# Performance work log

Measured on AMD Instinct MI355X. Metric: run time of the kernel, lower is better.

Reference implementation:

```python
import jax, jax.numpy as jnp
import numpy as np

NUM_HEADS = 16
HEAD_DIM = 64
D_MODEL = 1024
OUTPUT_DIM = 1024


def setup_inputs() -> dict:
    key = jax.random.key(0)
    ks = jax.random.split(key, 11)
    B, S, H = 2, 2048, D_MODEL
    inner = NUM_HEADS * HEAD_DIM
    s = 0.02
    return {
        "query": jax.random.normal(ks[0], (B, S, H), jnp.float32),
        "key": jax.random.normal(ks[1], (B, S, H), jnp.float32),
        "value": jax.random.normal(ks[2], (B, S, H), jnp.float32),
        "Wq": jax.random.normal(ks[3], (H, inner), jnp.float32) * s,
        "bq": jnp.zeros((inner,), jnp.float32),
        "Wk": jax.random.normal(ks[4], (H, inner), jnp.float32) * s,
        "bk": jnp.zeros((inner,), jnp.float32),
        "Wv": jax.random.normal(ks[5], (H, inner), jnp.float32) * s,
        "bv": jnp.zeros((inner,), jnp.float32),
        "Wo": jax.random.normal(ks[6], (inner, OUTPUT_DIM), jnp.float32) * s,
        "bo": jnp.zeros((OUTPUT_DIM,), jnp.float32),
    }


def reference(query, key, value, Wq, bq, Wk, bk, Wv, bv, Wo, bo):
    B, Sq, _ = query.shape
    Sk = key.shape[1]
    nh, dh = NUM_HEADS, HEAD_DIM
    # projections -> [B, S, nh, dh]
    Q = (query @ Wq + bq).reshape(B, Sq, nh, dh)
    K = (key @ Wk + bk).reshape(B, Sk, nh, dh)
    V = (value @ Wv + bv).reshape(B, Sk, nh, dh)
    # scores [B, nh, Sq, Sk]
    scores = jnp.einsum("bqhd,bkhd->bhqk", Q, K) / jnp.sqrt(jnp.float32(dh))
    attn = jax.nn.softmax(scores, axis=-1)
    out = jnp.einsum("bhqk,bkhd->bqhd", attn, V).reshape(B, Sq, nh * dh)
    return out @ Wo + bo
```

## Files before the change

kernel.cpp:

```cpp
#include <hip/hip_runtime.h>
#include <math.h>

typedef __attribute__((ext_vector_type(8))) short short8;
typedef __attribute__((ext_vector_type(4))) short short4v;
typedef __attribute__((ext_vector_type(4))) float f32x4;
typedef __attribute__((ext_vector_type(2))) float f32x2;

#if __has_builtin(__builtin_amdgcn_mfma_f32_16x16x16bf16_1k)
#define HAVE_MFMA16 1
#else
#define HAVE_MFMA16 0
#endif

__device__ __forceinline__ short f2bf(float f) {
  union { float f; unsigned u; } x; x.f = f;
  unsigned r = x.u + 0x7fffu + ((x.u >> 16) & 1u);
  return (short)(r >> 16);
}
#if __has_builtin(__builtin_amdgcn_cvt_pk_bf16_f32)
typedef __attribute__((ext_vector_type(2))) __bf16 bf16x2;
__device__ __forceinline__ unsigned pack_bf(float a, float b) {
  union { bf16x2 v; unsigned u; } t;
  t.v = __builtin_amdgcn_cvt_pk_bf16_f32(a, b);
  return t.u;
}
#else
__device__ __forceinline__ unsigned pack_bf(float a, float b) {
  union { float f; unsigned u; } x, y; x.f = a; y.f = b;
  unsigned ra = x.u + 0x7fffu + ((x.u >> 16) & 1u);
  unsigned rb = y.u + 0x7fffu + ((y.u >> 16) & 1u);
  return (ra >> 16) | (rb & 0xffff0000u);
}
#endif
__device__ __forceinline__ float fast_exp2(float x) {
#if __has_builtin(__builtin_amdgcn_exp2f)
  return __builtin_amdgcn_exp2f(x);
#else
  return exp2f(x);
#endif
}
union U4S8 { unsigned u[4]; short8 s; };
union U2S4 { unsigned u[2]; short4v s; };

__global__ __launch_bounds__(256) void wconv(
    const float* __restrict__ W0, const float* __restrict__ W1,
    const float* __restrict__ W2, const float* __restrict__ W3,
    short* __restrict__ T0, short* __restrict__ T1,
    short* __restrict__ T2, short* __restrict__ T3) {
  const float* W; short* T;
  switch (blockIdx.z) {
    case 0: W = W0; T = T0; break;
    case 1: W = W1; T = T1; break;
    case 2: W = W2; T = T2; break;
    default: W = W3; T = T3; break;
  }
  __shared__ __align__(16) short t[64][72];
  const int tid = threadIdx.x;
  const int x0 = blockIdx.x * 64, y0 = blockIdx.y * 64;
  {
    int rr = tid >> 2, cc = (tid & 3) * 16;
    const float* p = W + (size_t)(x0 + rr) * 1024 + y0 + cc;
    f32x4 v[4];
    v[0] = *(const f32x4*)(p + 0);  v[1] = *(const f32x4*)(p + 4);
    v[2] = *(const f32x4*)(p + 8);  v[3] = *(const f32x4*)(p + 12);
#pragma unroll
    for (int i = 0; i < 4; ++i)
#pragma unroll
      for (int j = 0; j < 4; ++j)
        t[cc + 4 * i + j][rr] = f2bf(v[i][j]);
  }
  __syncthreads();
  {
    int nr = tid >> 2, kc = (tid & 3) * 16;
    short* q = T + (size_t)(y0 + nr) * 1024 + x0 + kc;
    *(short8*)q       = *(const short8*)&t[nr][kc];
    *(short8*)(q + 8) = *(const short8*)&t[nr][kc + 8];
  }
}

template <bool A_IS_F32, bool B_IS_BF16, bool OUT_F32, int BM>
__global__ __launch_bounds__(256) void gemm_bias(
    const void* __restrict__ A0, const void* __restrict__ A1, const void* __restrict__ A2,
    const void* __restrict__ B0, const void* __restrict__ B1, const void* __restrict__ B2,
    const float* __restrict__ b0, const float* __restrict__ b1, const float* __restrict__ b2,
    void* __restrict__ C0, void* __restrict__ C1, void* __restrict__ C2,
    float s0, float s1, float s2, int M, int N, int K) {
  const int z = blockIdx.z;
  const void*  Av   = z == 0 ? A0 : (z == 1 ? A1 : A2);
  const void*  Bv   = z == 0 ? B0 : (z == 1 ? B1 : B2);
  const float* bias = z == 0 ? b0 : (z == 1 ? b1 : b2);
  void*        Cv   = z == 0 ? C0 : (z == 1 ? C1 : C2);
  const float  cs   = z == 0 ? s0 : (z == 1 ? s1 : s2);

  constexpr int MF = BM / 32;
  __shared__ __align__(16) short As[BM * 40];
  __shared__ __align__(16) short Bs[128 * 40];
  const int tid = threadIdx.x;
  const int l = tid & 63, w = tid >> 6;
  const int lr = l & 15, lq = l >> 4;
  const int lin = blockIdx.x + (int)gridDim.x * blockIdx.y;
  const int ny = (int)gridDim.y;
  const int yb = lin % ny, xb = lin / ny;
  const int m0 = yb * BM, n0 = xb * 128;
  const int wm = (w >> 1) * (BM / 2), wn = (w & 1) * 64;
  f32x4 acc[MF][4] = {};

  constexpr int TPR = 256 / BM;
  const int ar = tid / TPR, ac = (tid % TPR) * (32 / TPR);
  const int br = tid >> 1, bcc = (tid & 1) * 16;
  const int dp = tid & 63, kb = tid >> 6;

  f32x4 avf[MF];
  short8 avb[BM / 64 > 0 ? BM / 64 : 1];
  short8 bvb[2];
  f32x2 bvf[8];

  auto load_regs = [&](int k0) {
    if constexpr (A_IS_F32) {
      const float* Ap = (const float*)Av + (size_t)(m0 + ar) * K + k0 + ac;
#pragma unroll
      for (int i = 0; i < MF; ++i) avf[i] = *(const f32x4*)(Ap + 4 * i);
    } else {
      const short* Ap = (const short*)Av + (size_t)(m0 + ar) * K + k0 + ac;
#pragma unroll
      for (int i = 0; i < BM / 64; ++i) avb[i] = *(const short8*)(Ap + 8 * i);
    }
    if constexpr (B_IS_BF16) {
      const short* Bp = (const short*)Bv + (size_t)(n0 + br) * K + k0 + bcc;
      bvb[0] = *(const short8*)(Bp + 0);
      bvb[1] = *(const short8*)(Bp + 8);
    } else {
      const float* Bp = (const float*)Bv + (size_t)(k0 + kb * 8) * N + n0 + 2 * dp;
#pragma unroll
      for (int i = 0; i < 4; ++i) {
        bvf[2 * i]     = *(const f32x2*)(Bp + (size_t)(2 * i) * N);
        bvf[2 * i + 1] = *(const f32x2*)(Bp + (size_t)(2 * i + 1) * N);
      }
    }
  };
  auto write_lds = [&]() {
    if constexpr (A_IS_F32) {
#pragma unroll
      for (int j = 0; j < MF / 2; ++j) {
        U4S8 p;
        p.u[0] = pack_bf(avf[2 * j][0], avf[2 * j][1]);
        p.u[1] = pack_bf(avf[2 * j][2], avf[2 * j][3]);
        p.u[2] = pack_bf(avf[2 * j + 1][0], avf[2 * j + 1][1]);
        p.u[3] = pack_bf(avf[2 * j + 1][2], avf[2 * j + 1][3]);
        *(short8*)&As[ar * 40 + ac + 8 * j] = p.s;
      }
    } else {
#pragma unroll
      for (int j = 0; j < BM / 64; ++j)
        *(short8*)&As[ar * 40 + ac + 8 * j] = avb[j];
    }
    if constexpr (B_IS_BF16) {
      *(short8*)&Bs[br * 40 + bcc] = bvb[0];
      *(short8*)&Bs[br * 40 + bcc + 8] = bvb[1];
    } else {
      U4S8 lo, hi;
#pragma unroll
      for (int i = 0; i < 4; ++i) {
        lo.u[i] = pack_bf(bvf[2 * i][0], bvf[2 * i + 1][0]);
        hi.u[i] = pack_bf(bvf[2 * i][1], bvf[2 * i + 1][1]);
      }
      *(short8*)&Bs[(2 * dp) * 40 + kb * 8] = lo.s;
      *(short8*)&Bs[(2 * dp + 1) * 40 + kb * 8] = hi.s;
    }
  };

  load_regs(0);
  const int KT = K >> 5;
  for (int kt = 0; kt < KT; ++kt) {
    write_lds();
    __syncthreads();
    if (kt + 1 < KT) load_regs((kt + 1) * 32);

    short8 af[MF], bfr[4];
#pragma unroll
    for (int i = 0; i < MF; ++i)
      af[i] = *(const short8*)&As[(wm + i * 16 + lr) * 40 + lq * 8];
#pragma unroll
    for (int i = 0; i < 4; ++i)
      bfr[i] = *(const short8*)&Bs[(wn + i * 16 + lr) * 40 + lq * 8];
#pragma unroll
    for (int mi = 0; mi < MF; ++mi)
#pragma unroll
      for (int ni = 0; ni < 4; ++ni)
        acc[mi][ni] = __builtin_amdgcn_mfma_f32_16x16x32_bf16(af[mi], bfr[ni], acc[mi][ni], 0, 0, 0);
    __syncthreads();
  }

#pragma unroll
  for (int ni = 0; ni < 4; ++ni) {
    int gn = n0 + wn + ni * 16 + lr;
    float bv = bias[gn];
#pragma unroll
    for (int mi = 0; mi < MF; ++mi) {
      int gm = m0 + wm + mi * 16 + lq * 4;
#pragma unroll
      for (int r = 0; r < 4; ++r) {
        float val = (acc[mi][ni][r] + bv) * cs;
        if constexpr (OUT_F32)
          ((float*)Cv)[(size_t)(gm + r) * N + gn] = val;
        else
          ((short*)Cv)[(size_t)(gm + r) * N + gn] = f2bf(val);
      }
    }
  }
}

__global__ __launch_bounds__(256) void attn128(
    const short* __restrict__ Q, const short* __restrict__ K,
    const short* __restrict__ V, short* __restrict__ ctx) {
  __shared__ __align__(16) short Ks[64][72];
  __shared__ __align__(16) short Vt[64][72];
#if !HAVE_MFMA16
  __shared__ __align__(16) short Ps2[4][32][68];
#endif
  const int tid = threadIdx.x, l = tid & 63, w = tid >> 6;
  const int lr = l & 15, lq = l >> 4;
  const int lin = blockIdx.x + 16 * blockIdx.y;
  const int h = lin & 15, qblk = lin >> 4;
  const int b = blockIdx.z, q0 = qblk * 128;
  const size_t bh = (size_t)b * 2048 * 1024 + (size_t)h * 64;
  const short* Kg = K + bh;
  const short* Vg = V + bh;

  short8 qb[2][2];
#pragma unroll
  for (int qf = 0; qf < 2; ++qf)
#pragma unroll
    for (int ks = 0; ks < 2; ++ks)
      qb[qf][ks] = *(const short8*)&Q[bh + (size_t)(q0 + w * 32 + qf * 16 + lr) * 1024 + ks * 32 + lq * 8];

  f32x4 accO[4][2] = {};
  float lpart[2] = {0.f, 0.f};

  const int kr = tid >> 2, kc = (tid & 3) * 16;
  const int vdp = tid & 31, vkb = tid >> 5;

  short8 kv0, kv1;
  unsigned vu[8];
  auto load_kv = [&](int kt) {
    const short* Kp = &Kg[(size_t)(kt * 64 + kr) * 1024 + kc];
    kv0 = *(const short8*)(Kp + 0);
    kv1 = *(const short8*)(Kp + 8);
#pragma unroll
    for (int i = 0; i < 8; ++i)
      vu[i] = *(const unsigned*)&Vg[(size_t)(kt * 64 + vkb * 8 + i) * 1024 + vdp * 2];
  };
  auto write_kv = [&]() {
    *(short8*)&Ks[kr][kc] = kv0;
    *(short8*)&Ks[kr][kc + 8] = kv1;
    U4S8 lo, hi;
#pragma unroll
    for (int j = 0; j < 4; ++j) {
      lo.u[j] = (vu[2 * j] & 0xffffu) | (vu[2 * j + 1] << 16);
      hi.u[j] = (vu[2 * j] >> 16) | (vu[2 * j + 1] & 0xffff0000u);
    }
    *(short8*)&Vt[2 * vdp][vkb * 8] = lo.s;
    *(short8*)&Vt[2 * vdp + 1][vkb * 8] = hi.s;
  };

  load_kv(0);
  for (int kt = 0; kt < 32; ++kt) {
    write_kv();
    __syncthreads();
    if (kt + 1 < 32) load_kv(kt + 1);

    short8 ka[4][2];
#pragma unroll
    for (int ni = 0; ni < 4; ++ni)
#pragma unroll
      for (int ks = 0; ks < 2; ++ks)
        ka[ni][ks] = *(const short8*)&Ks[ni * 16 + lr][ks * 32 + lq * 8];
    f32x4 s[4][2] = {};
#pragma unroll
    for (int ni = 0; ni < 4; ++ni)
#pragma unroll
      for (int qf = 0; qf < 2; ++qf) {
        s[ni][qf] = __builtin_amdgcn_mfma_f32_16x16x32_bf16(ka[ni][0], qb[qf][0], s[ni][qf], 0, 0, 0);
        s[ni][qf] = __builtin_amdgcn_mfma_f32_16x16x32_bf16(ka[ni][1], qb[qf][1], s[ni][qf], 0, 0, 0);
      }

    unsigned pk[4][2][2];
#pragma unroll
    for (int ni = 0; ni < 4; ++ni)
#pragma unroll
      for (int qf = 0; qf < 2; ++qf) {
        float p0 = fast_exp2(s[ni][qf][0]);
        float p1 = fast_exp2(s[ni][qf][1]);
        float p2 = fast_exp2(s[ni][qf][2]);
        float p3 = fast_exp2(s[ni][qf][3]);
        lpart[qf] += (p0 + p1) + (p2 + p3);
        pk[ni][qf][0] = pack_bf(p0, p1);
        pk[ni][qf][1] = pack_bf(p2, p3);
      }

#if HAVE_MFMA16
#pragma unroll
    for (int di = 0; di < 4; ++di)
#pragma unroll
      for (int ni = 0; ni < 4; ++ni) {
        short4v vb = *(const short4v*)&Vt[di * 16 + lr][ni * 16 + lq * 4];
#pragma unroll
        for (int qf = 0; qf < 2; ++qf) {
          U2S4 a; a.u[0] = pk[ni][qf][0]; a.u[1] = pk[ni][qf][1];
          accO[di][qf] = __builtin_amdgcn_mfma_f32_16x16x16bf16_1k(a.s, vb, accO[di][qf], 0, 0, 0);
        }
      }
#else
#pragma unroll
    for (int ni = 0; ni < 4; ++ni)
#pragma unroll
      for (int qf = 0; qf < 2; ++qf) {
        unsigned* dst = (unsigned*)&Ps2[w][qf * 16 + lr][16 * ni + 4 * lq];
        dst[0] = pk[ni][qf][0];
        dst[1] = pk[ni][qf][1];
      }
#pragma unroll
    for (int ks = 0; ks < 2; ++ks)
#pragma unroll
      for (int qf = 0; qf < 2; ++qf) {
        const short* src = &Ps2[w][qf * 16 + lr][32 * ks + 8 * lq];
        U4S8 a;
        a.u[0] = ((const unsigned*)src)[0]; a.u[1] = ((const unsigned*)src)[1];
        a.u[2] = ((const unsigned*)src)[2]; a.u[3] = ((const unsigned*)src)[3];
#pragma unroll
        for (int di = 0; di < 4; ++di) {
          short8 vb = *(const short8*)&Vt[di * 16 + lr][ks * 32 + lq * 8];
          accO[di][qf] = __builtin_amdgcn_mfma_f32_16x16x32_bf16(a.s, vb, accO[di][qf], 0, 0, 0);
        }
      }
#endif
    __syncthreads();
  }

#pragma unroll
  for (int qf = 0; qf < 2; ++qf) {
    lpart[qf] += __shfl_xor(lpart[qf], 16, 64);
    lpart[qf] += __shfl_xor(lpart[qf], 32, 64);
  }
  float inv[2] = {1.0f / lpart[0], 1.0f / lpart[1]};
  float ir[2][4];
#pragma unroll
  for (int qf = 0; qf < 2; ++qf)
#pragma unroll
    for (int r = 0; r < 4; ++r)
      ir[qf][r] = __shfl(inv[qf], 4 * lq + r, 64);

#pragma unroll
  for (int qf = 0; qf < 2; ++qf)
#pragma unroll
    for (int r = 0; r < 4; ++r) {
      size_t row = bh + (size_t)(q0 + w * 32 + qf * 16 + 4 * lq + r) * 1024;
#pragma unroll
      for (int di = 0; di < 4; ++di)
        ctx[row + di * 16 + lr] = f2bf(accO[di][qf][r] * ir[qf][r]);
    }
}

extern "C" void kernel_launch(void* const* d_in, const int* in_sizes, int n_in,
                              void* d_out, int out_size, void* d_ws, size_t ws_size,
                              hipStream_t stream) {
  const void*  query = d_in[0];
  const void*  key   = d_in[1];
  const void*  value = d_in[2];
  const float* Wq = (const float*)d_in[3];
  const float* bq = (const float*)d_in[4];
  const float* Wk = (const float*)d_in[5];
  const float* bk = (const float*)d_in[6];
  const float* Wv = (const float*)d_in[7];
  const float* bv = (const float*)d_in[8];
  const float* Wo = (const float*)d_in[9];
  const float* bo = (const float*)d_in[10];

  short* ws = (short*)d_ws;
  const size_t MT = 4096ull * 1024ull;
  const size_t WSZ = 1024ull * 1024ull;
  short* Qb = ws;
  short* Vb = ws + MT;
  short* Kb = (short*)d_out;

  const bool roomy = ws_size >= (2 * MT + 4 * WSZ) * sizeof(short);
  short *WqT, *WkT, *WvT, *WoT;
  if (roomy) {
    short* base = ws + 2 * MT;
    WqT = base; WkT = base + WSZ; WvT = base + 2 * WSZ; WoT = base + 3 * WSZ;
  } else {
    short* tail = (short*)d_out + MT;
    WqT = tail; WkT = tail + WSZ; WvT = tail + 2 * WSZ; WoT = nullptr;
  }

  wconv<<<dim3(16, 16, roomy ? 4 : 3), 256, 0, stream>>>(
      Wq, Wk, Wv, Wo, WqT, WkT, WvT, roomy ? WoT : WvT);

  const float qscale = 0.125f * 1.4426950408889634f;
  gemm_bias<true, true, false, 128><<<dim3(8, 32, 3), 256, 0, stream>>>(
      query, key, value, WqT, WkT, WvT, bq, bk, bv, Qb, Kb, Vb,
      qscale, 1.0f, 1.0f, 4096, 1024, 1024);

  attn128<<<dim3(16, 16, 2), 256, 0, stream>>>(Qb, Kb, Vb, Qb );

  if (roomy)
    gemm_bias<false, true, true, 64><<<dim3(8, 64, 1), 256, 0, stream>>>(
        Qb, Qb, Qb, WoT, WoT, WoT, bo, bo, bo, d_out, d_out, d_out,
        1.0f, 1.0f, 1.0f, 4096, 1024, 1024);
  else
    gemm_bias<false, false, true, 64><<<dim3(8, 64, 1), 256, 0, stream>>>(
        Qb, Qb, Qb, Wo, Wo, Wo, bo, bo, bo, d_out, d_out, d_out,
        1.0f, 1.0f, 1.0f, 4096, 1024, 1024);
}
```

Measured before the change: 253.5 us.

## Pre-convert activations to bf16 and use async global-to-LDS GEMM loads

When the workspace is large enough, a new pass converts the query, key and value activations from fp32 to bf16 up front. New GEMMs then stream bf16 tiles straight from global memory into LDS using global_load_lds and run 16x16x32 bf16 MFMAs. The goal is to remove the per-tile fp32 conversion and register staging from the projection GEMM's inner loop. The cost is an extra launch and extra traffic to write and re-read bf16 copies of the activations, and the loop is still single-buffered with two barriers per k-step.

```diff
diff --git a/kernel.cpp b/kernel.cpp
--- a/kernel.cpp
+++ b/kernel.cpp
@@ -41,6 +41,12 @@
 }
 union U4S8 { unsigned u[4]; short8 s; };
 union U2S4 { unsigned u[2]; short4v s; };
+
+__device__ __forceinline__ void async16(const short* g, short* lds_uniform) {
+  __builtin_amdgcn_global_load_lds(
+      (const __attribute__((address_space(1))) void*)g,
+      (__attribute__((address_space(3))) void*)lds_uniform, 16, 0, 0);
+}
 
 __global__ __launch_bounds__(256) void wconv(
     const float* __restrict__ W0, const float* __restrict__ W1,
@@ -75,6 +81,118 @@
     short* q = T + (size_t)(y0 + nr) * 1024 + x0 + kc;
     *(short8*)q       = *(const short8*)&t[nr][kc];
     *(short8*)(q + 8) = *(const short8*)&t[nr][kc + 8];
+  }
+}
+
+__global__ __launch_bounds__(256) void aconv(
+    const float* __restrict__ X0, const float* __restrict__ X1, const float* __restrict__ X2,
+    short* __restrict__ Y0, short* __restrict__ Y1, short* __restrict__ Y2) {
+  const float* X; short* Y;
+  switch (blockIdx.z) {
+    case 0: X = X0; Y = Y0; break;
+    case 1: X = X1; Y = Y1; break;
+    default: X = X2; Y = Y2; break;
+  }
+  size_t idx = ((size_t)blockIdx.x * 256 + threadIdx.x) * 16;
+  f32x4 v0 = *(const f32x4*)(X + idx + 0);
+  f32x4 v1 = *(const f32x4*)(X + idx + 4);
+  f32x4 v2 = *(const f32x4*)(X + idx + 8);
+  f32x4 v3 = *(const f32x4*)(X + idx + 12);
+  U4S8 a, b;
+  a.u[0] = pack_bf(v0[0], v0[1]); a.u[1] = pack_bf(v0[2], v0[3]);
+  a.u[2] = pack_bf(v1[0], v1[1]); a.u[3] = pack_bf(v1[2], v1[3]);
+  b.u[0] = pack_bf(v2[0], v2[1]); b.u[1] = pack_bf(v2[2], v2[3]);
+  b.u[2] = pack_bf(v3[0], v3[1]); b.u[3] = pack_bf(v3[2], v3[3]);
+  *(short8*)(Y + idx) = a.s;
+  *(short8*)(Y + idx + 8) = b.s;
+}
+
+template <bool OUT_F32, int BM>
+__global__ __launch_bounds__(256) void gemm_async(
+    const short* __restrict__ A0, const short* __restrict__ A1, const short* __restrict__ A2,
+    const short* __restrict__ B0, const short* __restrict__ B1, const short* __restrict__ B2,
+    const float* __restrict__ b0, const float* __restrict__ b1, const float* __restrict__ b2,
+    void* __restrict__ C0, void* __restrict__ C1, void* __restrict__ C2,
+    float s0, float s1, float s2, int M, int N, int K) {
+  const int z = blockIdx.z;
+  const short* A    = z == 0 ? A0 : (z == 1 ? A1 : A2);
+  const short* B    = z == 0 ? B0 : (z == 1 ? B1 : B2);
+  const float* bias = z == 0 ? b0 : (z == 1 ? b1 : b2);
+  void*        Cv   = z == 0 ? C0 : (z == 1 ? C1 : C2);
+  const float  cs   = z == 0 ? s0 : (z == 1 ? s1 : s2);
+
+  constexpr int MF = BM / 32;
+  constexpr int AJ = BM / 64;
+  __shared__ __align__(16) short As[BM * 32];
+  __shared__ __align__(16) short Bs[128 * 32];
+  const int tid = threadIdx.x;
+  const int l = tid & 63, w = tid >> 6;
+  const int lr = l & 15, lq = l >> 4;
+  const int lin = blockIdx.x + (int)gridDim.x * blockIdx.y;
+  const int ny = (int)gridDim.y;
+  const int yb = lin % ny, xb = lin / ny;
+  const int m0 = yb * BM, n0 = xb * 128;
+  const int wm = (w >> 1) * (BM / 2), wn = (w & 1) * 64;
+  f32x4 acc[MF][4] = {};
+
+  const int lrow = l >> 2, lcol = (l & 3) * 8;
+  const short* aptr[AJ];
+  short* alds[AJ];
+#pragma unroll
+  for (int j = 0; j < AJ; ++j) {
+    int chunk = w * AJ + j;
+    aptr[j] = A + (size_t)(m0 + chunk * 16 + lrow) * K + lcol;
+    alds[j] = &As[chunk * 512];
+  }
+  const short* bptr[2];
+  short* blds[2];
+#pragma unroll
+  for (int j = 0; j < 2; ++j) {
+    int chunk = w * 2 + j;
+    bptr[j] = B + (size_t)(n0 + chunk * 16 + lrow) * K + lcol;
+    blds[j] = &Bs[chunk * 512];
+  }
+
+  const int KT = K >> 5;
+  for (int kt = 0; kt < KT; ++kt) {
+    const int k0 = kt * 32;
+    __syncthreads();
+#pragma unroll
+    for (int j = 0; j < AJ; ++j) async16(aptr[j] + k0, alds[j]);
+#pragma unroll
+    for (int j = 0; j < 2; ++j) async16(bptr[j] + k0, blds[j]);
+    __syncthreads();
+
+    short8 af[MF], bfr[4];
+#pragma unroll
+    for (int i = 0; i < MF; ++i)
+      af[i] = *(const short8*)&As[(wm + i * 16 + lr) * 32 + lq * 8];
+#pragma unroll
+    for (int i = 0; i < 4; ++i)
+      bfr[i] = *(const short8*)&Bs[(wn + i * 16 + lr) * 32 + lq * 8];
+#pragma unroll
+    for (int mi = 0; mi < MF; ++mi)
+#pragma unroll
+      for (int ni = 0; ni < 4; ++ni)
+        acc[mi][ni] = __builtin_amdgcn_mfma_f32_16x16x32_bf16(af[mi], bfr[ni], acc[mi][ni], 0, 0, 0);
+  }
+
+#pragma unroll
+  for (int ni = 0; ni < 4; ++ni) {
+    int gn = n0 + wn + ni * 16 + lr;
+    float bv = bias[gn];
+#pragma unroll
+    for (int mi = 0; mi < MF; ++mi) {
+      int gm = m0 + wm + mi * 16 + lq * 4;
+#pragma unroll
+      for (int r = 0; r < 4; ++r) {
+        float val = (acc[mi][ni][r] + bv) * cs;
+        if constexpr (OUT_F32)
+          ((float*)Cv)[(size_t)(gm + r) * N + gn] = val;
+        else
+          ((short*)Cv)[(size_t)(gm + r) * N + gn] = f2bf(val);
+      }
+    }
   }
 }
 
@@ -379,9 +497,35 @@
   short* ws = (short*)d_ws;
   const size_t MT = 4096ull * 1024ull;
   const size_t WSZ = 1024ull * 1024ull;
+  const float qscale = 0.125f * 1.4426950408889634f;
+
   short* Qb = ws;
   short* Vb = ws + MT;
   short* Kb = (short*)d_out;
+
+  const bool turbo = ws_size >= (4 * MT + 4 * WSZ) * sizeof(short);
+
+  if (turbo) {
+    short* Qcv = ws + 2 * MT;
+    short* Vcv = ws + 3 * MT;
+    short* Kcv = (short*)d_out + MT;
+    short* WqT = ws + 4 * MT;
+    short* WkT = WqT + WSZ;
+    short* WvT = WqT + 2 * WSZ;
+    short* WoT = WqT + 3 * WSZ;
+
+    wconv<<<dim3(16, 16, 4), 256, 0, stream>>>(Wq, Wk, Wv, Wo, WqT, WkT, WvT, WoT);
+    aconv<<<dim3(1024, 1, 3), 256, 0, stream>>>(
+        (const float*)query, (const float*)key, (const float*)value, Qcv, Kcv, Vcv);
+    gemm_async<false, 128><<<dim3(8, 32, 3), 256, 0, stream>>>(
+        Qcv, Kcv, Vcv, WqT, WkT, WvT, bq, bk, bv, Qb, Kb, Vb,
+        qscale, 1.0f, 1.0f, 4096, 1024, 1024);
+    attn128<<<dim3(16, 16, 2), 256, 0, stream>>>(Qb, Kb, Vb, Qb);
+    gemm_async<true, 64><<<dim3(8, 64, 1), 256, 0, stream>>>(
+        Qb, Qb, Qb, WoT, WoT, WoT, bo, bo, bo, d_out, d_out, d_out,
+        1.0f, 1.0f, 1.0f, 4096, 1024, 1024);
+    return;
+  }
 
   const bool roomy = ws_size >= (2 * MT + 4 * WSZ) * sizeof(short);
   short *WqT, *WkT, *WvT, *WoT;
@@ -396,12 +540,11 @@
   wconv<<<dim3(16, 16, roomy ? 4 : 3), 256, 0, stream>>>(
       Wq, Wk, Wv, Wo, WqT, WkT, WvT, roomy ? WoT : WvT);
 
-  const float qscale = 0.125f * 1.4426950408889634f;
   gemm_bias<true, true, false, 128><<<dim3(8, 32, 3), 256, 0, stream>>>(
       query, key, value, WqT, WkT, WvT, bq, bk, bv, Qb, Kb, Vb,
       qscale, 1.0f, 1.0f, 4096, 1024, 1024);
 
-  attn128<<<dim3(16, 16, 2), 256, 0, stream>>>(Qb, Kb, Vb, Qb );
+  attn128<<<dim3(16, 16, 2), 256, 0, stream>>>(Qb, Kb, Vb, Qb);
 
   if (roomy)
     gemm_bias<false, true, true, 64><<<dim3(8, 64, 1), 256, 0, stream>>>(
```

Result: faster. 240.3 us (-5.2%).
